# Optimization experiments

Measured on AMD Instinct MI355X. Metric: run time of the kernel, lower is better.

The kernel has to match this reference:

```python
import jax, jax.numpy as jnp
import numpy as np

INF = 10000000000000.0
HEADS = 12
HEAD_SIZE = 64

def _rope_tables(seqlen, dim):
    inv_freq = 1.0 / (10000.0 ** (jnp.arange(0, dim, 2, dtype=jnp.float32) / dim))
    t = jnp.arange(seqlen, dtype=jnp.float32)
    freqs = t[:, None] * inv_freq[None, :]            # [S, d/2]
    # unsqueeze_dim=-2 -> [S, 1, d/2] to broadcast over heads
    return jnp.sin(freqs)[:, None, :], jnp.cos(freqs)[:, None, :]

def _apply_rope(t, sin, cos):
    # t: [B, S, H, D]; sin/cos: [S, 1, D/2]
    t1, t2 = t[..., 0::2], t[..., 1::2]
    out = jnp.stack([t1 * cos - t2 * sin, t1 * sin + t2 * cos], axis=-1)
    return out.reshape(t.shape)

def setup_inputs() -> dict:
    key = jax.random.key(0)
    k1, k2 = jax.random.split(key)
    B, S, Hd = 32, 512, 1024
    x = jax.random.normal(k1, (B, S, Hd), dtype=jnp.float32)
    W = jax.random.normal(k2, (Hd, HEADS * 2 * HEAD_SIZE), dtype=jnp.float32) * (1.0 / np.sqrt(Hd))
    b = jnp.zeros((HEADS * 2 * HEAD_SIZE,), dtype=jnp.float32)
    attention_mask = jnp.ones((B, S), dtype=jnp.int32)
    return {"x": x, "W": W, "b": b, "attention_mask": attention_mask}

def reference(x, W, b, attention_mask):
    B, S, _ = x.shape
    proj = x @ W + b                                   # [B, S, H*2*D]
    proj = proj.reshape(B, S, HEADS, 2, HEAD_SIZE)
    qw, kw = proj[..., 0, :], proj[..., 1, :]          # [B, S, H, D]
    sin, cos = _rope_tables(S, HEAD_SIZE)
    qw = _apply_rope(qw, sin, cos)
    kw = _apply_rope(kw, sin, cos)
    logits = jnp.einsum('bmhd,bnhd->bhmn', qw, kw)     # [B, H, S, S]
    am = attention_mask.astype(logits.dtype)
    pad_mask = 1.0 - am[:, None, None, :] * am[:, None, :, None]
    logits = logits - pad_mask * INF
    idx = jnp.arange(S)
    tril = (idx[:, None] > idx[None, :]).astype(logits.dtype)  # strictly lower triangle
    logits = logits - tril * INF
    return logits / (HEAD_SIZE ** 0.5)
```

## Files before the change

### kernel.cpp

```cpp
#include <hip/hip_runtime.h>
#include <hip/hip_bf16.h>
#include <cstdint>

#define HEADS 12
#define HEAD_SIZE 64
#define SEQ 512
#define HD 1024
#define NPROJ 1536
#define INF_VAL 1e13f

typedef __attribute__((ext_vector_type(8))) __bf16 bf16x8;
typedef __attribute__((ext_vector_type(4))) float f32x4;

__device__ __forceinline__ unsigned short f2bf(float f) {
    unsigned u = __float_as_uint(f);
    u += 0x7fffu + ((u >> 16) & 1u);
    return (unsigned short)(u >> 16);
}

__global__ void __launch_bounds__(256) transpose_cast_w(const float* __restrict__ W,
                                                        unsigned short* __restrict__ Wt) {
    __shared__ unsigned short tile[64][65];
    const int bx = blockIdx.x;
    const int k0 = (bx & 15) * 64;
    const int n0 = (bx >> 4) * 64;
    const int t = threadIdx.x;
    const int tr = t >> 4;
    const int tc = (t & 15) * 4;
#pragma unroll
    for (int i = 0; i < 4; ++i) {
        int kk = tr + i * 16;
        float4 v = *(const float4*)&W[(size_t)(k0 + kk) * NPROJ + n0 + tc];
        tile[kk][tc + 0] = f2bf(v.x);
        tile[kk][tc + 1] = f2bf(v.y);
        tile[kk][tc + 2] = f2bf(v.z);
        tile[kk][tc + 3] = f2bf(v.w);
    }
    __syncthreads();
#pragma unroll
    for (int i = 0; i < 4; ++i) {
        int nn = tr + i * 16;
        ushort4 o;
        o.x = tile[tc + 0][nn];
        o.y = tile[tc + 1][nn];
        o.z = tile[tc + 2][nn];
        o.w = tile[tc + 3][nn];
        *(ushort4*)&Wt[(size_t)(n0 + nn) * HD + k0 + tc] = o;
    }
}

__global__ void __launch_bounds__(256) gemm1_rope(const float* __restrict__ x,
                                                  const unsigned short* __restrict__ Wt,
                                                  const float* __restrict__ bias,
                                                  unsigned short* __restrict__ qws,
                                                  unsigned short* __restrict__ kws) {
    __shared__ __align__(16) char smem[32768];
    unsigned short* Alds = (unsigned short*)smem;
    unsigned short* Blds = (unsigned short*)(smem + 10240);

    const int bx = blockIdx.x;
    const int tile_m = bx / HEADS;
    const int h = bx - tile_m * HEADS;
    const int m0 = tile_m * 128;
    const int n0 = h * 128;

    const int t = threadIdx.x;
    const int w = t >> 6;
    const int lane = t & 63;
    const int wm = w >> 1;
    const int wn = w & 1;
    const int c16 = lane & 15;
    const int quad = lane >> 4;

    const int sr = t >> 1;
    const int sc = (t & 1) * 16;

    f32x4 acc[4][4];
#pragma unroll
    for (int i = 0; i < 4; ++i)
#pragma unroll
        for (int j = 0; j < 4; ++j) acc[i][j] = (f32x4){0.f, 0.f, 0.f, 0.f};

    const float* xrow = x + (size_t)(m0 + sr) * HD + sc;
    const unsigned short* wrow = Wt + (size_t)(n0 + sr) * HD + sc;

    for (int kt = 0; kt < HD; kt += 32) {
        float4 v0 = *(const float4*)(xrow + kt + 0);
        float4 v1 = *(const float4*)(xrow + kt + 4);
        float4 v2 = *(const float4*)(xrow + kt + 8);
        float4 v3 = *(const float4*)(xrow + kt + 12);
        uint4 p0, p1;
        p0.x = f2bf(v0.x) | ((unsigned)f2bf(v0.y) << 16);
        p0.y = f2bf(v0.z) | ((unsigned)f2bf(v0.w) << 16);
        p0.z = f2bf(v1.x) | ((unsigned)f2bf(v1.y) << 16);
        p0.w = f2bf(v1.z) | ((unsigned)f2bf(v1.w) << 16);
        p1.x = f2bf(v2.x) | ((unsigned)f2bf(v2.y) << 16);
        p1.y = f2bf(v2.z) | ((unsigned)f2bf(v2.w) << 16);
        p1.z = f2bf(v3.x) | ((unsigned)f2bf(v3.y) << 16);
        p1.w = f2bf(v3.z) | ((unsigned)f2bf(v3.w) << 16);
        *(uint4*)((char*)Alds + sr * 80 + sc * 2) = p0;
        *(uint4*)((char*)Alds + sr * 80 + sc * 2 + 16) = p1;
        const uint4* bsrc = (const uint4*)(wrow + kt);
        *(uint4*)((char*)Blds + sr * 80 + sc * 2) = bsrc[0];
        *(uint4*)((char*)Blds + sr * 80 + sc * 2 + 16) = bsrc[1];
        __syncthreads();

        bf16x8 af[4], bfr[4];
#pragma unroll
        for (int mi = 0; mi < 4; ++mi)
            af[mi] = *(const bf16x8*)((char*)Alds + (wm * 64 + mi * 16 + c16) * 80 + quad * 16);
#pragma unroll
        for (int ni = 0; ni < 4; ++ni)
            bfr[ni] = *(const bf16x8*)((char*)Blds + (wn * 64 + ni * 16 + c16) * 80 + quad * 16);
#pragma unroll
        for (int mi = 0; mi < 4; ++mi)
#pragma unroll
            for (int ni = 0; ni < 4; ++ni)
                acc[mi][ni] = __builtin_amdgcn_mfma_f32_16x16x32_bf16(af[mi], bfr[ni], acc[mi][ni], 0, 0, 0);
        __syncthreads();
    }

    float bv[4];
#pragma unroll
    for (int ni = 0; ni < 4; ++ni) bv[ni] = bias[n0 + wn * 64 + ni * 16 + c16];

    float2* tab = (float2*)smem;
    const int sbase = m0 & (SEQ - 1);
#pragma unroll
    for (int i = 0; i < 16; ++i) {
        int e = t * 16 + i;
        int srow = e >> 5;
        int fi = e & 31;
        float invf = __expf(-(float)fi * (0.03125f * 9.210340371976184f));
        float theta = (float)(sbase + srow) * invf;
        float sv, cv;
        __sincosf(theta, &sv, &cv);
        tab[e] = make_float2(sv, cv);
    }
    __syncthreads();

    unsigned short* outp = wn ? kws : qws;
#pragma unroll
    for (int mi = 0; mi < 4; ++mi) {
#pragma unroll
        for (int ni = 0; ni < 4; ++ni) {
            int d = ni * 16 + c16;
            int fi = d >> 1;
            float sgn = (d & 1) ? 1.f : -1.f;
#pragma unroll
            for (int r = 0; r < 4; ++r) {
                float v = acc[mi][ni][r] + bv[ni];
                float p = __shfl_xor(v, 1, 64);
                int srow = wm * 64 + mi * 16 + quad * 4 + r;
                float2 sc2 = tab[srow * 32 + fi];
                float o = v * sc2.y + sgn * p * sc2.x;
                int m = m0 + srow;
                int bb = m >> 9;
                int ss = m & (SEQ - 1);
                outp[((size_t)(bb * HEADS + h) * SEQ + ss) * HEAD_SIZE + d] = f2bf(o);
            }
        }
    }
}

__global__ void __launch_bounds__(256) gemm2_mask(const unsigned short* __restrict__ qws,
                                                  const unsigned short* __restrict__ kws,
                                                  const int* __restrict__ am,
                                                  float* __restrict__ out) {
    __shared__ __align__(16) unsigned short qlds[128 * 72];
    __shared__ __align__(16) unsigned short klds[128 * 72];
    const int bh = blockIdx.y;
    const int b = bh / HEADS;
    const int tm = (blockIdx.x >> 2) * 128;
    const int tn = (blockIdx.x & 3) * 128;
    const int t = threadIdx.x;
    const int w = t >> 6, lane = t & 63;
    const int wm = w >> 1, wn = w & 1;
    const int c16 = lane & 15, quad = lane >> 4;

    {
        const int sr = t >> 1;
        const int sc = (t & 1) * 32;
        const uint4* src = (const uint4*)(qws + ((size_t)bh * SEQ + tm + sr) * HEAD_SIZE + sc);
        uint4* dst = (uint4*)((char*)qlds + sr * 144 + sc * 2);
        dst[0] = src[0]; dst[1] = src[1]; dst[2] = src[2]; dst[3] = src[3];
        const uint4* src2 = (const uint4*)(kws + ((size_t)bh * SEQ + tn + sr) * HEAD_SIZE + sc);
        uint4* dst2 = (uint4*)((char*)klds + sr * 144 + sc * 2);
        dst2[0] = src2[0]; dst2[1] = src2[1]; dst2[2] = src2[2]; dst2[3] = src2[3];
    }
    __syncthreads();

    f32x4 acc[4][4];
#pragma unroll
    for (int i = 0; i < 4; ++i)
#pragma unroll
        for (int j = 0; j < 4; ++j) acc[i][j] = (f32x4){0.f, 0.f, 0.f, 0.f};

#pragma unroll
    for (int ks = 0; ks < 2; ++ks) {
        bf16x8 af[4], bfr[4];
#pragma unroll
        for (int mi = 0; mi < 4; ++mi)
            af[mi] = *(const bf16x8*)((char*)qlds + (wm * 64 + mi * 16 + c16) * 144 + ks * 64 + quad * 16);
#pragma unroll
        for (int ni = 0; ni < 4; ++ni)
            bfr[ni] = *(const bf16x8*)((char*)klds + (wn * 64 + ni * 16 + c16) * 144 + ks * 64 + quad * 16);
#pragma unroll
        for (int mi = 0; mi < 4; ++mi)
#pragma unroll
            for (int ni = 0; ni < 4; ++ni)
                acc[mi][ni] = __builtin_amdgcn_mfma_f32_16x16x32_bf16(af[mi], bfr[ni], acc[mi][ni], 0, 0, 0);
    }

    const int* amb = am + b * SEQ;
    float amn[4];
#pragma unroll
    for (int ni = 0; ni < 4; ++ni) amn[ni] = (float)amb[tn + wn * 64 + ni * 16 + c16];
#pragma unroll
    for (int mi = 0; mi < 4; ++mi) {
#pragma unroll
        for (int r = 0; r < 4; ++r) {
            int m = tm + wm * 64 + mi * 16 + quad * 4 + r;
            float amm = (float)amb[m];
#pragma unroll
            for (int ni = 0; ni < 4; ++ni) {
                int n = tn + wn * 64 + ni * 16 + c16;
                float pen = (1.0f - amm * amn[ni]) + ((m > n) ? 1.0f : 0.0f);
                out[((size_t)bh * SEQ + m) * SEQ + n] = (acc[mi][ni][r] - pen * INF_VAL) * 0.125f;
            }
        }
    }
}

extern "C" void kernel_launch(void* const* d_in, const int* in_sizes, int n_in,
                              void* d_out, int out_size, void* d_ws, size_t ws_size,
                              hipStream_t stream) {
    (void)in_sizes; (void)n_in; (void)out_size; (void)ws_size;
    const float* x = (const float*)d_in[0];
    const float* W = (const float*)d_in[1];
    const float* bias = (const float*)d_in[2];
    const int* am = (const int*)d_in[3];
    float* out = (float*)d_out;

    unsigned short* Wt = (unsigned short*)d_ws;
    unsigned short* qws = (unsigned short*)((char*)d_ws + 3145728);
    unsigned short* kws = (unsigned short*)((char*)d_ws + 3145728 + 25165824);

    hipLaunchKernelGGL(transpose_cast_w, dim3(384), dim3(256), 0, stream, W, Wt);
    hipLaunchKernelGGL(gemm1_rope, dim3(128 * HEADS), dim3(256), 0, stream, x, Wt, bias, qws, kws);
    hipLaunchKernelGGL(gemm2_mask, dim3(16, 32 * HEADS), dim3(256), 0, stream, qws, kws, am, out);
}
```

Baseline: 587.5 us.

## Pre-convert x to bf16 and stage GEMM tiles via direct global-to-LDS loads

Adds a separate kernel that converts x to bf16 once into workspace, so the projection GEMM no longer reloads fp32 x and repeats the conversion for each of the 12 head tiles. The GEMM main loop now uses global_load_lds to move 16-byte bf16 chunks straight into LDS, bypassing registers, with an unpadded 64-byte row stride. This cuts global traffic and VALU work in the GEMM. In exchange it adds an extra pass writing and reading a bf16 copy of x, and the unpadded LDS layout may cause bank conflicts on fragment reads.

Result: faster. 549.4 us (-6.5%).

```diff
diff --git a/kernel.cpp b/kernel.cpp
--- a/kernel.cpp
+++ b/kernel.cpp
@@ -16,6 +16,26 @@
     unsigned u = __float_as_uint(f);
     u += 0x7fffu + ((u >> 16) & 1u);
     return (unsigned short)(u >> 16);
+}
+
+__device__ __forceinline__ void gl_lds16(const unsigned short* g, unsigned short* l) {
+    __builtin_amdgcn_global_load_lds(
+        (const __attribute__((address_space(1))) unsigned int*)g,
+        (__attribute__((address_space(3))) unsigned int*)l, 16, 0, 0);
+}
+
+__global__ void __launch_bounds__(256) convert_x(const float* __restrict__ x,
+                                                 unsigned short* __restrict__ xb) {
+    const int i = blockIdx.x * 256 + threadIdx.x;
+    const float4* src = (const float4*)x;
+    float4 v0 = src[i * 2 + 0];
+    float4 v1 = src[i * 2 + 1];
+    uint4 p;
+    p.x = f2bf(v0.x) | ((unsigned)f2bf(v0.y) << 16);
+    p.y = f2bf(v0.z) | ((unsigned)f2bf(v0.w) << 16);
+    p.z = f2bf(v1.x) | ((unsigned)f2bf(v1.y) << 16);
+    p.w = f2bf(v1.z) | ((unsigned)f2bf(v1.w) << 16);
+    ((uint4*)xb)[i] = p;
 }
 
 __global__ void __launch_bounds__(256) transpose_cast_w(const float* __restrict__ W,
@@ -49,14 +69,14 @@
     }
 }
 
-__global__ void __launch_bounds__(256) gemm1_rope(const float* __restrict__ x,
+__global__ void __launch_bounds__(256) gemm1_rope(const unsigned short* __restrict__ xb,
                                                   const unsigned short* __restrict__ Wt,
                                                   const float* __restrict__ bias,
                                                   unsigned short* __restrict__ qws,
                                                   unsigned short* __restrict__ kws) {
     __shared__ __align__(16) char smem[32768];
     unsigned short* Alds = (unsigned short*)smem;
-    unsigned short* Blds = (unsigned short*)(smem + 10240);
+    unsigned short* Blds = (unsigned short*)(smem + 8192);
 
     const int bx = blockIdx.x;
     const int tile_m = bx / HEADS;
@@ -72,8 +92,16 @@
     const int c16 = lane & 15;
     const int quad = lane >> 4;
 
-    const int sr = t >> 1;
-    const int sc = (t & 1) * 16;
+    const int row0 = w * 32 + (lane >> 2);
+    const int celem = (lane & 3) * 8;
+    const unsigned short* ga0 = xb + (size_t)(m0 + row0) * HD + celem;
+    const unsigned short* ga1 = xb + (size_t)(m0 + row0 + 16) * HD + celem;
+    const unsigned short* gb0 = Wt + (size_t)(n0 + row0) * HD + celem;
+    const unsigned short* gb1 = Wt + (size_t)(n0 + row0 + 16) * HD + celem;
+    unsigned short* la0 = Alds + row0 * 32 + celem;
+    unsigned short* la1 = Alds + (row0 + 16) * 32 + celem;
+    unsigned short* lb0 = Blds + row0 * 32 + celem;
+    unsigned short* lb1 = Blds + (row0 + 16) * 32 + celem;
 
     f32x4 acc[4][4];
 #pragma unroll
@@ -81,37 +109,20 @@
 #pragma unroll
         for (int j = 0; j < 4; ++j) acc[i][j] = (f32x4){0.f, 0.f, 0.f, 0.f};
 
-    const float* xrow = x + (size_t)(m0 + sr) * HD + sc;
-    const unsigned short* wrow = Wt + (size_t)(n0 + sr) * HD + sc;
-
     for (int kt = 0; kt < HD; kt += 32) {
-        float4 v0 = *(const float4*)(xrow + kt + 0);
-        float4 v1 = *(const float4*)(xrow + kt + 4);
-        float4 v2 = *(const float4*)(xrow + kt + 8);
-        float4 v3 = *(const float4*)(xrow + kt + 12);
-        uint4 p0, p1;
-        p0.x = f2bf(v0.x) | ((unsigned)f2bf(v0.y) << 16);
-        p0.y = f2bf(v0.z) | ((unsigned)f2bf(v0.w) << 16);
-        p0.z = f2bf(v1.x) | ((unsigned)f2bf(v1.y) << 16);
-        p0.w = f2bf(v1.z) | ((unsigned)f2bf(v1.w) << 16);
-        p1.x = f2bf(v2.x) | ((unsigned)f2bf(v2.y) << 16);
-        p1.y = f2bf(v2.z) | ((unsigned)f2bf(v2.w) << 16);
-        p1.z = f2bf(v3.x) | ((unsigned)f2bf(v3.y) << 16);
-        p1.w = f2bf(v3.z) | ((unsigned)f2bf(v3.w) << 16);
-        *(uint4*)((char*)Alds + sr * 80 + sc * 2) = p0;
-        *(uint4*)((char*)Alds + sr * 80 + sc * 2 + 16) = p1;
-        const uint4* bsrc = (const uint4*)(wrow + kt);
-        *(uint4*)((char*)Blds + sr * 80 + sc * 2) = bsrc[0];
-        *(uint4*)((char*)Blds + sr * 80 + sc * 2 + 16) = bsrc[1];
+        gl_lds16(ga0 + kt, la0);
+        gl_lds16(ga1 + kt, la1);
+        gl_lds16(gb0 + kt, lb0);
+        gl_lds16(gb1 + kt, lb1);
         __syncthreads();
 
         bf16x8 af[4], bfr[4];
 #pragma unroll
         for (int mi = 0; mi < 4; ++mi)
-            af[mi] = *(const bf16x8*)((char*)Alds + (wm * 64 + mi * 16 + c16) * 80 + quad * 16);
+            af[mi] = *(const bf16x8*)((char*)Alds + (wm * 64 + mi * 16 + c16) * 64 + quad * 16);
 #pragma unroll
         for (int ni = 0; ni < 4; ++ni)
-            bfr[ni] = *(const bf16x8*)((char*)Blds + (wn * 64 + ni * 16 + c16) * 80 + quad * 16);
+            bfr[ni] = *(const bf16x8*)((char*)Blds + (wn * 64 + ni * 16 + c16) * 64 + quad * 16);
 #pragma unroll
         for (int mi = 0; mi < 4; ++mi)
 #pragma unroll
@@ -242,11 +253,13 @@
     const int* am = (const int*)d_in[3];
     float* out = (float*)d_out;
 
-    unsigned short* Wt = (unsigned short*)d_ws;
+    unsigned short* Wt  = (unsigned short*)d_ws;
     unsigned short* qws = (unsigned short*)((char*)d_ws + 3145728);
     unsigned short* kws = (unsigned short*)((char*)d_ws + 3145728 + 25165824);
-
+    unsigned short* xb  = (unsigned short*)((char*)d_ws + 3145728 + 2 * 25165824);
+
+    hipLaunchKernelGGL(convert_x, dim3(8192), dim3(256), 0, stream, x, xb);
     hipLaunchKernelGGL(transpose_cast_w, dim3(384), dim3(256), 0, stream, W, Wt);
-    hipLaunchKernelGGL(gemm1_rope, dim3(128 * HEADS), dim3(256), 0, stream, x, Wt, bias, qws, kws);
+    hipLaunchKernelGGL(gemm1_rope, dim3(128 * HEADS), dim3(256), 0, stream, xb, Wt, bias, qws, kws);
     hipLaunchKernelGGL(gemm2_mask, dim3(16, 32 * HEADS), dim3(256), 0, stream, qws, kws, am, out);
 }
```
